# Optimization experiments

Measured on AMD Instinct MI355X. Metric: run time of the kernel, lower is better.

## Reference

```python
import jax, jax.numpy as jnp
import numpy as np

N = 2_000_000
H, W = 50, 50
BIRTH_RANGE = (0.0, 1.0)
PERS_RANGE = (0.0, 1.0)
EPS = 1e-08


def setup_inputs() -> dict:
    key = jax.random.key(0)
    k1, = jax.random.split(key, 1)
    # (birth, death) pairs in [0,1); math is identical regardless of death>=birth
    pairs = jax.random.uniform(k1, (N, 2), dtype=jnp.float32)
    sigma = jnp.float32(0.1)  # learnable scalar parameter
    grid_x = jnp.linspace(BIRTH_RANGE[0], BIRTH_RANGE[1], W, dtype=jnp.float32)
    grid_y = jnp.linspace(PERS_RANGE[0], PERS_RANGE[1], H, dtype=jnp.float32)
    return {"pairs": pairs, "sigma": sigma, "grid_x": grid_x, "grid_y": grid_y}


def reference(pairs, sigma, grid_x, grid_y):
    birth = pairs[:, 0]
    pers = pairs[:, 1] - pairs[:, 0]
    # normalize into grid coordinates (default ranges are (0,1))
    birth_norm = (birth - BIRTH_RANGE[0]) / (BIRTH_RANGE[1] - BIRTH_RANGE[0] + EPS)
    pers_norm = (pers - PERS_RANGE[0]) / (PERS_RANGE[1] - PERS_RANGE[0] + EPS)
    weights = pers  # weight_fn == 'linear'
    inv2s2 = 1.0 / (2.0 * sigma * sigma)
    # separable Gaussian splat: [N, W] and [N, H]
    gx = jnp.exp(-((grid_x[None, :] - birth_norm[:, None]) ** 2) * inv2s2)
    gy = jnp.exp(-((grid_y[None, :] - pers_norm[:, None]) ** 2) * inv2s2)
    # sum_i w_i * outer(gy_i, gx_i), without materializing [N, H, W]
    image = jnp.einsum('n,nh,nw->hw', weights, gy, gx)
    return image / (image.max() + EPS)
```

## Files before the change

### kernel.cpp

```cpp
#include <hip/hip_runtime.h>

#define HH 50
#define WW 50
#define EPSF 1e-8f

#define BXH 160
#define BYH 240
#define Y0F (-0.5f)
#define YSPAN 1.5f
#define REPSZ (BXH * BYH)

#define GXOFF 0
#define GYOFF (GXOFF + WW * BXH)
#define POFF  (GYOFF + HH * BYH)
#define REPOFF (POFF + BYH * WW)

__device__ __forceinline__ unsigned bf16pk(float a, float b) {
    unsigned ua = __float_as_uint(a), ub = __float_as_uint(b);
    ua = (ua + 0x7FFFu + ((ua >> 16) & 1u)) >> 16;
    ub = (ub + 0x7FFFu + ((ub >> 16) & 1u)) >> 16;
    return ua | (ub << 16);
}

__device__ __forceinline__ void splat1(float b, float death, float* hist) {
    const float p = death - b;
    if (p < Y0F) return;
    int ix = (int)(b * (float)BXH);
    int iy = (int)((p - Y0F) * ((float)BYH / YSPAN));
    ix = min(ix, BXH - 1);
    iy = min(iy, BYH - 1);
    atomicAdd(&hist[iy * BXH + ix], p);
}

__global__ __launch_bounds__(1024) void pie_hist_lds(
    const float4* __restrict__ pairs4, int n,
    const float* __restrict__ grid_x, const float* __restrict__ grid_y,
    const float* __restrict__ sigma_p, float* __restrict__ ws, int R)
{
    __shared__ float hist[REPSZ];
    const int t = threadIdx.x;

    for (int i = t; i < REPSZ; i += 1024) hist[i] = 0.0f;

    if (blockIdx.x == 0) {
        const float s = *sigma_p;
        const float a = 1.0f / (2.0f * s * s);
        for (int i = t; i < WW * BXH; i += 1024) {
            const int w = i / BXH, ix = i - w * BXH;
            const float c = (ix + 0.5f) * (1.0f / BXH);
            const float d = grid_x[w] - c;
            ws[GXOFF + i] = __expf(-d * d * a);
        }
        for (int i = t; i < HH * BYH; i += 1024) {
            const int h = i / BYH, iy = i - h * BYH;
            const float c = Y0F + (iy + 0.5f) * (YSPAN / (float)BYH);
            const float d = grid_y[h] - c;
            ws[GYOFF + i] = __expf(-d * d * a);
        }
    }
    __syncthreads();

    const int n2 = n >> 1;
    const int stride = R * 1024;
    #pragma unroll 2
    for (int i = blockIdx.x * 1024 + t; i < n2; i += stride) {
        const float4 q = pairs4[i];
        splat1(q.x, q.y, hist);
        splat1(q.z, q.w, hist);
    }
    if ((n & 1) && blockIdx.x == 0 && t == 0) {
        const float2 last = ((const float2*)pairs4)[n - 1];
        splat1(last.x, last.y, hist);
    }
    __syncthreads();

    uint2* dst = (uint2*)((char*)(ws + REPOFF) + (size_t)blockIdx.x * (REPSZ * 2));
    const float4* src = (const float4*)hist;
    for (int i = t; i < REPSZ / 4; i += 1024) {
        const float4 v = src[i];
        uint2 o;
        o.x = bf16pk(v.x, v.y);
        o.y = bf16pk(v.z, v.w);
        dst[i] = o;
    }
}

__global__ __launch_bounds__(1024) void pie_c1(float* __restrict__ ws, int R)
{
    __shared__ float part[12 * BXH];
    __shared__ float row[BXH];
    __shared__ float gxl[WW * (BXH + 1)];
    const int t = threadIdx.x;
    const int rowi = blockIdx.x;

    for (int i = t; i < WW * BXH; i += 1024) {
        const int w = i / BXH, ix = i - w * BXH;
        gxl[w * (BXH + 1) + ix] = ws[GXOFF + i];
    }

    const int r0 = t / 80;
    const int px = t - r0 * 80;
    if (r0 < 12) {
        const unsigned* repu = (const unsigned*)((char*)(ws + REPOFF)) + rowi * 80 + px;
        float alo = 0.0f, ahi = 0.0f;
        #pragma unroll 4
        for (int r = r0; r < R; r += 12) {
            const unsigned u = repu[(size_t)r * (REPSZ / 2)];
            alo += __uint_as_float(u << 16);
            ahi += __uint_as_float(u & 0xFFFF0000u);
        }
        part[r0 * BXH + 2 * px]     = alo;
        part[r0 * BXH + 2 * px + 1] = ahi;
    }
    __syncthreads();

    if (t < BXH) {
        float s = 0.0f;
        #pragma unroll
        for (int k = 0; k < 12; ++k) s += part[k * BXH + t];
        row[t] = s;
    }
    __syncthreads();

    if (t < WW) {
        float acc = 0.0f;
        #pragma unroll 4
        for (int k = 0; k < BXH; ++k)
            acc += row[k] * gxl[t * (BXH + 1) + k];
        ws[POFF + rowi * WW + t] = acc;
    }
}

__global__ __launch_bounds__(1024) void pie_c2(const float* __restrict__ ws,
                                               float* __restrict__ out)
{
    __shared__ float gyl[HH * BYH];
    __shared__ float Pl[BYH * WW];
    __shared__ float img[HH * WW];
    __shared__ float wmax[16];
    const int t = threadIdx.x;

    for (int i = t; i < HH * BYH; i += 1024) gyl[i] = ws[GYOFF + i];
    for (int i = t; i < BYH * WW; i += 1024) Pl[i] = ws[POFF + i];
    __syncthreads();

    for (int c = t; c < HH * WW; c += 1024) {
        const int h = c / WW, w = c - h * WW;
        float acc = 0.0f;
        #pragma unroll 4
        for (int r = 0; r < BYH; ++r)
            acc += gyl[h * BYH + r] * Pl[r * WW + w];
        img[c] = acc;
    }
    __syncthreads();

    float m = -1e30f;
    for (int c = t; c < HH * WW; c += 1024) m = fmaxf(m, img[c]);
    #pragma unroll
    for (int off = 32; off > 0; off >>= 1)
        m = fmaxf(m, __shfl_down(m, off));
    const int wv = t >> 6, ln = t & 63;
    if (ln == 0) wmax[wv] = m;
    __syncthreads();
    if (t == 0) {
        float mm = wmax[0];
        for (int k = 1; k < 16; ++k) mm = fmaxf(mm, wmax[k]);
        wmax[0] = mm;
    }
    __syncthreads();

    const float inv = 1.0f / (wmax[0] + EPSF);
    for (int c = t; c < HH * WW; c += 1024) out[c] = img[c] * inv;
}

extern "C" void kernel_launch(void* const* d_in, const int* in_sizes, int n_in,
                              void* d_out, int out_size, void* d_ws, size_t ws_size,
                              hipStream_t stream) {
    const float4* pairs4 = (const float4*)d_in[0];
    const float*  sigma  = (const float*)d_in[1];
    const float*  grid_x = (const float*)d_in[2];
    const float*  grid_y = (const float*)d_in[3];
    float* ws  = (float*)d_ws;
    float* out = (float*)d_out;
    const int n = in_sizes[0] / 2;

    const long avail_bytes = (long)ws_size - (long)REPOFF * 4;
    long cap = avail_bytes / (REPSZ * 2);
    int R = (int)(cap < 256 ? cap : 256);
    if (R < 1) R = 1;

    pie_hist_lds<<<R, 1024, 0, stream>>>(pairs4, n, grid_x, grid_y, sigma, ws, R);
    pie_c1<<<BYH, 1024, 0, stream>>>(ws, R);
    pie_c2<<<1, 1024, 0, stream>>>(ws, out);
}
```

Measured before the change: 115.5 us.

## Parallelize final contraction across blocks with last-block max normalization

The final gy·P contraction, which ran on one block, is split across 50 blocks, one per output row. Each block writes its image row to workspace, and a global atomic counter picks the last block to do the max reduction and normalization. The c1 reduction also moves to 640 threads reading 8-byte bf16 packs with 16 replica groups, which widens loads. The change adds a threadfence/counter protocol and a counter reset inside the histogram kernel.

```diff
diff --git a/kernel.cpp b/kernel.cpp
--- a/kernel.cpp
+++ b/kernel.cpp
@@ -13,7 +13,9 @@
 #define GXOFF 0
 #define GYOFF (GXOFF + WW * BXH)
 #define POFF  (GYOFF + HH * BYH)
-#define REPOFF (POFF + BYH * WW)
+#define IMGOFF (POFF + BYH * WW)
+#define CNTOFF (IMGOFF + HH * WW + 12)
+#define REPOFF (CNTOFF + 4)
 
 __device__ __forceinline__ unsigned bf16pk(float a, float b) {
     unsigned ua = __float_as_uint(a), ub = __float_as_uint(b);
@@ -43,6 +45,7 @@
     for (int i = t; i < REPSZ; i += 1024) hist[i] = 0.0f;
 
     if (blockIdx.x == 0) {
+        if (t == 0) ((int*)ws)[CNTOFF] = 0;
         const float s = *sigma_p;
         const float a = 1.0f / (2.0f * s * s);
         for (int i = t; i < WW * BXH; i += 1024) {
@@ -74,7 +77,7 @@
     }
     __syncthreads();
 
-    uint2* dst = (uint2*)((char*)(ws + REPOFF) + (size_t)blockIdx.x * (REPSZ * 2));
+    uint2* dst = (uint2*)((char*)ws + (size_t)REPOFF * 4 + (size_t)blockIdx.x * (REPSZ * 2));
     const float4* src = (const float4*)hist;
     for (int i = t; i < REPSZ / 4; i += 1024) {
         const float4 v = src[i];
@@ -85,40 +88,42 @@
     }
 }
 
-__global__ __launch_bounds__(1024) void pie_c1(float* __restrict__ ws, int R)
+__global__ __launch_bounds__(640) void pie_c1(float* __restrict__ ws, int R)
 {
-    __shared__ float part[12 * BXH];
+    __shared__ float part[16 * BXH];
     __shared__ float row[BXH];
     __shared__ float gxl[WW * (BXH + 1)];
     const int t = threadIdx.x;
     const int rowi = blockIdx.x;
 
-    for (int i = t; i < WW * BXH; i += 1024) {
+    for (int i = t; i < WW * BXH; i += 640) {
         const int w = i / BXH, ix = i - w * BXH;
         gxl[w * (BXH + 1) + ix] = ws[GXOFF + i];
     }
 
-    const int r0 = t / 80;
-    const int px = t - r0 * 80;
-    if (r0 < 12) {
-        const unsigned* repu = (const unsigned*)((char*)(ws + REPOFF)) + rowi * 80 + px;
-        float alo = 0.0f, ahi = 0.0f;
+    const int g = t / 40;
+    const int s = t - g * 40;
+    {
+        const char* repbase = (const char*)ws + (size_t)REPOFF * 4;
+        float a0 = 0.0f, a1 = 0.0f, a2 = 0.0f, a3 = 0.0f;
         #pragma unroll 4
-        for (int r = r0; r < R; r += 12) {
-            const unsigned u = repu[(size_t)r * (REPSZ / 2)];
-            alo += __uint_as_float(u << 16);
-            ahi += __uint_as_float(u & 0xFFFF0000u);
+        for (int r = g; r < R; r += 16) {
+            const uint2 u = *(const uint2*)(repbase + (size_t)r * (REPSZ * 2)
+                                            + (size_t)(rowi * 40 + s) * 8);
+            a0 += __uint_as_float(u.x << 16);
+            a1 += __uint_as_float(u.x & 0xFFFF0000u);
+            a2 += __uint_as_float(u.y << 16);
+            a3 += __uint_as_float(u.y & 0xFFFF0000u);
         }
-        part[r0 * BXH + 2 * px]     = alo;
-        part[r0 * BXH + 2 * px + 1] = ahi;
+        ((float4*)part)[g * 40 + s] = make_float4(a0, a1, a2, a3);
     }
     __syncthreads();
 
     if (t < BXH) {
-        float s = 0.0f;
+        float sum = 0.0f;
         #pragma unroll
-        for (int k = 0; k < 12; ++k) s += part[k * BXH + t];
-        row[t] = s;
+        for (int k = 0; k < 16; ++k) sum += part[k * BXH + t];
+        row[t] = sum;
     }
     __syncthreads();
 
@@ -131,46 +136,55 @@
     }
 }
 
-__global__ __launch_bounds__(1024) void pie_c2(const float* __restrict__ ws,
-                                               float* __restrict__ out)
+__global__ __launch_bounds__(256) void pie_c2(float* __restrict__ ws,
+                                              float* __restrict__ out)
 {
-    __shared__ float gyl[HH * BYH];
-    __shared__ float Pl[BYH * WW];
-    __shared__ float img[HH * WW];
-    __shared__ float wmax[16];
+    __shared__ float part[5 * WW];
+    __shared__ float redmax[4];
+    __shared__ int is_last;
+    const int h = blockIdx.x;
     const int t = threadIdx.x;
 
-    for (int i = t; i < HH * BYH; i += 1024) gyl[i] = ws[GYOFF + i];
-    for (int i = t; i < BYH * WW; i += 1024) Pl[i] = ws[POFF + i];
-    __syncthreads();
-
-    for (int c = t; c < HH * WW; c += 1024) {
-        const int h = c / WW, w = c - h * WW;
+    if (t < 5 * WW) {
+        const int w = t % WW;
+        const int c = t / WW;
+        const float* gy = ws + GYOFF + h * BYH;
+        const float* P  = ws + POFF;
+        const int r0 = c * (BYH / 5);
         float acc = 0.0f;
         #pragma unroll 4
-        for (int r = 0; r < BYH; ++r)
-            acc += gyl[h * BYH + r] * Pl[r * WW + w];
-        img[c] = acc;
-    }
-    __syncthreads();
+        for (int r = r0; r < r0 + BYH / 5; ++r)
+            acc += gy[r] * P[r * WW + w];
+        part[t] = acc;
+    }
+    __syncthreads();
+    if (t < WW)
+        ws[IMGOFF + h * WW + t] = part[t] + part[WW + t] + part[2 * WW + t]
+                                + part[3 * WW + t] + part[4 * WW + t];
+    __threadfence();
+    __syncthreads();
+    if (t == 0) {
+        const int old = atomicAdd((int*)ws + CNTOFF, 1);
+        is_last = (old == HH - 1);
+    }
+    __syncthreads();
+    if (!is_last) return;
+    __threadfence();
 
     float m = -1e30f;
-    for (int c = t; c < HH * WW; c += 1024) m = fmaxf(m, img[c]);
+    for (int i = t; i < HH * WW; i += 256) m = fmaxf(m, ws[IMGOFF + i]);
     #pragma unroll
     for (int off = 32; off > 0; off >>= 1)
         m = fmaxf(m, __shfl_down(m, off));
     const int wv = t >> 6, ln = t & 63;
-    if (ln == 0) wmax[wv] = m;
-    __syncthreads();
-    if (t == 0) {
-        float mm = wmax[0];
-        for (int k = 1; k < 16; ++k) mm = fmaxf(mm, wmax[k]);
-        wmax[0] = mm;
-    }
-    __syncthreads();
-
-    const float inv = 1.0f / (wmax[0] + EPSF);
-    for (int c = t; c < HH * WW; c += 1024) out[c] = img[c] * inv;
+    if (ln == 0) redmax[wv] = m;
+    __syncthreads();
+    if (t == 0)
+        redmax[0] = fmaxf(fmaxf(redmax[0], redmax[1]), fmaxf(redmax[2], redmax[3]));
+    __syncthreads();
+
+    const float inv = 1.0f / (redmax[0] + EPSF);
+    for (int i = t; i < HH * WW; i += 256) out[i] = ws[IMGOFF + i] * inv;
 }
 
 extern "C" void kernel_launch(void* const* d_in, const int* in_sizes, int n_in,
@@ -190,6 +204,6 @@
     if (R < 1) R = 1;
 
     pie_hist_lds<<<R, 1024, 0, stream>>>(pairs4, n, grid_x, grid_y, sigma, ws, R);
-    pie_c1<<<BYH, 1024, 0, stream>>>(ws, R);
-    pie_c2<<<1, 1024, 0, stream>>>(ws, out);
-}
+    pie_c1<<<BYH, 640, 0, stream>>>(ws, R);
+    pie_c2<<<HH, 256, 0, stream>>>(ws, out);
+}
```

After: 107.1 us. -7.2%, faster.
